# Optimization experiments

Hardware: AMD Instinct MI355X
Metric: run time of the kernel (lower is better)

Reference implementation:

```python
import jax, jax.numpy as jnp
import numpy as np
import math

B, T, XD, H, DD, P = 512, 256, 128, 512, 16, 32
IN = 2 * XD + DD  # GRUCell input size


def _init(key, shape, fan):
    stdv = 1.0 / math.sqrt(fan)
    return jax.random.uniform(key, shape, jnp.float32, -stdv, stdv)


def setup_inputs() -> dict:
    key = jax.random.key(0)
    ks = jax.random.split(key, 32)
    inp = {
        "values": jax.random.normal(ks[0], (B, T, XD), jnp.float32),
        "lens": jnp.full((B,), T, dtype=jnp.int32),  # lens[0] == max_len
        "static": jax.random.normal(ks[1], (B, DD), jnp.float32),
        "times": jax.random.uniform(ks[2], (B, T, XD), jnp.float32),
        "masks": (jax.random.uniform(ks[3], (B, T, XD)) < 0.8).astype(jnp.float32),
        "prototype": jax.random.normal(ks[4], (P, H), jnp.float32),
        "proto": True,
        # temp_decay_h: Linear(x_dim -> hidden), custom uniform(-1/sqrt(H), 1/sqrt(H))
        "Wd": _init(ks[5], (H, XD), H), "bd": _init(ks[6], (H,), XD),
        # hist_reg: Linear(hidden -> x_dim)
        "Wh": _init(ks[7], (XD, H), H), "bh": _init(ks[8], (XD,), H),
        "Wf": _init(ks[9], (XD, XD), XD), "bf": _init(ks[10], (XD,), XD),
        # ProtoAttn Q/K/V: Linear(hidden -> hidden)
        "Wq": _init(ks[11], (H, H), H), "bq": _init(ks[12], (H,), H),
        "Wk": _init(ks[13], (H, H), H), "bk": _init(ks[14], (H,), H),
        "Wv": _init(ks[15], (H, H), H), "bv": _init(ks[16], (H,), H),
        # gating W: Linear(2*hidden -> 1)
        "Wg": _init(ks[17], (1, 2 * H), 2 * H), "bg": _init(ks[18], (1,), 2 * H),
        # GRUCell
        "Wih": _init(ks[19], (3 * H, IN), H), "Whh": _init(ks[20], (3 * H, H), H),
        "bih": _init(ks[21], (3 * H,), H), "bhh": _init(ks[22], (3 * H,), H),
    }
    return inp


def _forward(values, static, times, masks, prototype,
             Wd, bd, Wh, bh, Wf, bf, Wq, bq, Wk, bk, Wv, bv, Wg, bg,
             Wih, Whh, bih, bhh, lens, proto):
    feat_m = 1.0 - jnp.eye(XD, dtype=values.dtype)  # zero-diagonal mask
    gamma = jnp.exp(-jax.nn.relu(jnp.einsum("btx,hx->bth", times, Wd) + bd))
    # attention key/value do not depend on h -> precompute
    keyp = prototype @ Wk.T + bk      # [P,H]
    valp = prototype @ Wv.T + bv      # [P,H]
    scale = 1.0 / math.sqrt(P)
    valid = (jnp.arange(T)[:, None] < lens[None, :]).astype(values.dtype)  # [T,B]

    xs = (jnp.swapaxes(values, 0, 1),  # [T,B,XD]
          jnp.swapaxes(masks, 0, 1),   # [T,B,XD]
          jnp.swapaxes(gamma, 0, 1),   # [T,B,H]
          valid[:, :, None])           # [T,B,1]

    h0 = jnp.zeros((B, H), values.dtype)
    xh0 = jnp.zeros((B, XD), values.dtype)

    def step(carry, xt):
        h, x_h = carry
        x, m, g, v = xt
        if proto:
            q = h @ Wq.T + bq                          # [B,H]
            score = (q @ keyp.T) * scale               # [B,P]
            attn = jax.nn.softmax(score, axis=-1)      # dropout omitted (eval)
            h1 = attn @ valp                           # [B,H]
            alpha = jax.nn.sigmoid(jnp.concatenate([h, h1], axis=1) @ Wg.T + bg)
            h = alpha * h + (1.0 - alpha) * h1
        h = h * g
        x_h = jnp.where(v > 0, h @ Wh.T + bh, x_h)
        x_c = m * x + (1.0 - m) * x_h
        z_h = x_c @ (Wf * feat_m).T + bf
        z_c = m * x + (1.0 - m) * z_h
        inp = jnp.concatenate([z_c, m, static], axis=1)
        gx = inp @ Wih.T + bih
        gh = h @ Whh.T + bhh
        xr, xz, xn = jnp.split(gx, 3, axis=1)
        hr, hz, hn = jnp.split(gh, 3, axis=1)
        r = jax.nn.sigmoid(xr + hr)
        z = jax.nn.sigmoid(xz + hz)
        n = jnp.tanh(xn + r * hn)
        h_new = (1.0 - z) * n + z * h
        h = jnp.where(v > 0, h_new, h)
        return (h, x_h), (h, x_c, z_c)

    (hN, _), (hs, x_cs, z_cs) = jax.lax.scan(step, (h0, xh0), xs)
    hs = jnp.swapaxes(hs, 0, 1)
    x_cs = jnp.swapaxes(x_cs, 0, 1)
    z_cs = jnp.swapaxes(z_cs, 0, 1)
    return hs, hN, x_cs, z_cs


def reference(values, lens, static, times, masks, prototype, proto,
              Wd, bd, Wh, bh, Wf, bf, Wq, bq, Wk, bk, Wv, bv, Wg, bg,
              Wih, Whh, bih, bhh):
    return _forward(values, static, times, masks, prototype,
                    Wd, bd, Wh, bh, Wf, bf, Wq, bq, Wk, bk, Wv, bv, Wg, bg,
                    Wih, Whh, bih, bhh, lens, bool(proto))
```

## Files before the change

kernel.cpp:

```cpp
#include <hip/hip_runtime.h>

#define NB 256
#define NT 1024

#define Bv 512
#define Tv 256
#define XDv 128
#define Hv 512
#define DDv 16
#define Pv 32

typedef short s8 __attribute__((ext_vector_type(8)));
typedef float f4 __attribute__((ext_vector_type(4)));
typedef unsigned long long u64;

#define OFF_KEYP 2048
#define OFF_VALP (OFF_KEYP + 16384)
#define OFF_MF   (OFF_VALP + 16384)
#define OFF_C    (OFF_MF + 16384)
#define OFF_VWG  (OFF_C + 32)
#define OFF_FRG  (OFF_VWG + 32)
#define US_WD   0
#define US_MS   65536
#define US_VP   81920
#define US_WH   98304
#define US_WF   163840
#define US_WHH  180224
#define US_WIH  966656
#define US_END  1409024
#define OFF_H   (OFF_FRG + (US_END/2))

#define OUT_HS  0
#define OUT_HN  (Bv*Tv*Hv)
#define OUT_XCS (OUT_HN + Bv*Hv)
#define OUT_ZCS (OUT_XCS + Bv*Tv*XDv)

struct Smem {
  unsigned short hA[32*520];
  unsigned short tA[32*136];
  unsigned short xcA[32*136];
  unsigned short inpA[32*296];
  unsigned short aA[32*40];
  unsigned short mA[32*136];
  unsigned short xhS[32*128];
  float xvS[32*132];
  float scS[32*34];
  float ghS[3*32*33];
  float gxS[3*32*33];
  float hp32[32*32];
  float al[32], rsm[32], cS[32], vwgS[32];
};

__device__ __forceinline__ unsigned short f2b(float f) {
  union { float f; unsigned int u; } x{f};
  unsigned int r = x.u + 0x7fffu + ((x.u >> 16) & 1u);
  return (unsigned short)(r >> 16);
}
__device__ __forceinline__ float b2f(unsigned short u) {
  union { unsigned int u; float f; } x{(unsigned int)u << 16};
  return x.f;
}
__device__ __forceinline__ float sig_f(float x) { return 1.f / (1.f + __expf(-x)); }
__device__ __forceinline__ float tanh_f(float x) {
  x = fminf(fmaxf(x, -15.f), 15.f);
  float e = __expf(2.f * x);
  return (e - 1.f) / (e + 1.f);
}
__device__ __forceinline__ s8 pack8(const float* p) {
  f4 a = *(const f4*)p; f4 b = *(const f4*)(p + 4);
  s8 r;
  r[0]=(short)f2b(a[0]); r[1]=(short)f2b(a[1]); r[2]=(short)f2b(a[2]); r[3]=(short)f2b(a[3]);
  r[4]=(short)f2b(b[0]); r[5]=(short)f2b(b[1]); r[6]=(short)f2b(b[2]); r[7]=(short)f2b(b[3]);
  return r;
}

__device__ __forceinline__ void gridbar(unsigned int* bar, unsigned int& lgen, int bid) {
  __syncthreads();
  if (threadIdx.x == 0) {
    __threadfence();
    const unsigned int target = ++lgen;
    unsigned int* grp = bar + (bid >> 4)*16;
    const unsigned int a =
        __hip_atomic_fetch_add(grp, 1u, __ATOMIC_ACQ_REL, __HIP_MEMORY_SCOPE_AGENT);
    if (a == 15u) {
      __hip_atomic_store(grp, 0u, __ATOMIC_RELAXED, __HIP_MEMORY_SCOPE_AGENT);
      const unsigned int r =
          __hip_atomic_fetch_add(bar + 384, 1u, __ATOMIC_ACQ_REL, __HIP_MEMORY_SCOPE_AGENT);
      if (r == 15u) {
        __hip_atomic_store(bar + 384, 0u, __ATOMIC_RELAXED, __HIP_MEMORY_SCOPE_AGENT);
        __hip_atomic_store(bar + 400, target, __ATOMIC_RELEASE, __HIP_MEMORY_SCOPE_AGENT);
      }
    }
    while (__hip_atomic_load(bar + 400, __ATOMIC_RELAXED, __HIP_MEMORY_SCOPE_AGENT) < target)
      __builtin_amdgcn_s_sleep(2);
    __threadfence();
  }
  __syncthreads();
}

__device__ __forceinline__ void rgbar_nf(unsigned int* bar, unsigned int& lgen, int rg) {
  __syncthreads();
  if (threadIdx.x == 0) {
    const unsigned int target = ++lgen;
    unsigned int* cnt = bar + 512 + rg*64;
    unsigned int* flg = cnt + 32;
    const unsigned int a =
        __hip_atomic_fetch_add(cnt, 1u, __ATOMIC_RELAXED, __HIP_MEMORY_SCOPE_AGENT);
    if (a == 15u) {
      __hip_atomic_store(cnt, 0u, __ATOMIC_RELAXED, __HIP_MEMORY_SCOPE_AGENT);
      asm volatile("s_waitcnt vmcnt(0)" ::: "memory");
      __hip_atomic_store(flg, target, __ATOMIC_RELAXED, __HIP_MEMORY_SCOPE_AGENT);
    } else {
      while (__hip_atomic_load(flg, __ATOMIC_RELAXED, __HIP_MEMORY_SCOPE_AGENT) < target)
        __builtin_amdgcn_s_sleep(2);
    }
  }
  __syncthreads();
}

#define SWZ(DST, NTILES, KT_, EXPR)                                            \
  { const int tot = (NTILES)*(KT_)*512;                                        \
    for (int f = gtid; f < tot; f += NB*NT) {                                  \
      const int e = f & 7, lane_ = (f >> 3) & 63, rem = f >> 9;                \
      const int kt = rem % (KT_), nt = rem / (KT_);                            \
      const int n = nt*16 + (lane_ & 15);                                      \
      const int k = kt*32 + ((lane_ >> 4) & 3)*8 + e;                          \
      (DST)[f] = f2b((EXPR));                                                  \
    } }

#define MFMA(a,b,c) __builtin_amdgcn_mfma_f32_16x16x32_bf16((a),(b),(c),0,0,0)
#define FRAG(P,idx) (*(const s8*)&(P)[((size_t)(idx))*8])
#define NTST(v,p) __builtin_nontemporal_store((v),(p))

__global__ __launch_bounds__(NT, 4)
void rits_main(const float* __restrict__ values, const int* __restrict__ lens,
               const float* __restrict__ statc, const float* __restrict__ times,
               const float* __restrict__ masks, const float* __restrict__ prototype,
               const int* __restrict__ protoflag,
               const float* __restrict__ Wd, const float* __restrict__ bd,
               const float* __restrict__ Wh, const float* __restrict__ bh,
               const float* __restrict__ Wf, const float* __restrict__ bf,
               const float* __restrict__ Wq, const float* __restrict__ bq,
               const float* __restrict__ Wk, const float* __restrict__ bk,
               const float* __restrict__ Wv, const float* __restrict__ bv,
               const float* __restrict__ Wg, const float* __restrict__ bg,
               const float* __restrict__ Wih, const float* __restrict__ Whh,
               const float* __restrict__ bih, const float* __restrict__ bhh,
               float* __restrict__ out, float* __restrict__ ws)
{
  const int bid = blockIdx.x, tid = threadIdx.x;
  const int gtid = bid*NT + tid;
  const int wv = tid >> 6, ln = tid & 63;
  const int l15 = ln & 15, l4 = ln >> 4;
  const int rg = (bid & 7)*2 + ((bid >> 7) & 1);
  const int cg = (bid >> 3) & 15;
  const int r0 = rg*32, c0 = cg*32;
  unsigned int* bar = (unsigned int*)ws;
  unsigned int lgenG = 0, lgenR = 0;
  unsigned short* frg = (unsigned short*)(ws + OFF_FRG);
  const unsigned short* wdW  = frg + US_WD;
  const unsigned short* msW  = frg + US_MS;
  const unsigned short* vpW  = frg + US_VP;
  const unsigned short* whW  = frg + US_WH;
  const unsigned short* wfW  = frg + US_WF;
  const unsigned short* whhW = frg + US_WHH;
  const unsigned short* wihW = frg + US_WIH;
  unsigned int* wsH = (unsigned int*)(ws + OFF_H);

  __shared__ Smem L;
  const bool proto = protoflag[0] != 0;
  const float scale = 0.17677669529663687f;

  for (int o = gtid; o < 2*Pv*Hv; o += NB*NT) {
    const int which = o >> 14, rem = o & 16383;
    const int p = rem >> 9, j = rem & 511;
    const float* W = which ? Wv : Wk;
    const float* bb = which ? bv : bk;
    const float* pr = prototype + p*Hv;
    const float* wr = W + j*Hv;
    float s = bb[j];
    #pragma unroll 4
    for (int k = 0; k < Hv; ++k) s += pr[k]*wr[k];
    ws[(which ? OFF_VALP : OFF_KEYP) + p*Hv + j] = s;
  }
  SWZ(frg + US_WD, 32, 4,  Wd[n*XDv + k])
  SWZ(frg + US_WH, 8, 16,  Wh[n*Hv + k])
  SWZ(frg + US_WF, 8, 4,   (n == k ? 0.f : Wf[n*XDv + k]))
  SWZ(frg + US_WHH, 96, 16,
      Whh[((size_t)(n >> 9)*Hv + (((n >> 5) & 15)*32 + ((n >> 4) & 1)*16 + (n & 15)))*Hv + k])
  SWZ(frg + US_WIH, 96, 9,
      (k < 272 ? Wih[((size_t)(n >> 9)*Hv + (((n >> 5) & 15)*32 + ((n >> 4) & 1)*16 + (n & 15)))*272 + k] : 0.f))
  gridbar(bar, lgenG, bid);

  {
    const float* keyp = ws + OFF_KEYP;
    const float* valp = ws + OFF_VALP;
    for (int o = gtid; o < Pv*Hv; o += NB*NT) {
      const int p = o >> 9, kc = o & 511;
      float s = 0.f;
      #pragma unroll 4
      for (int j = 0; j < Hv; ++j) s += keyp[p*Hv + j]*Wq[j*Hv + kc];
      ws[OFF_MF + o] = s;
    }
    if (gtid < 32) {
      float s = 0.f;
      for (int j = 0; j < Hv; ++j) s += bq[j]*keyp[gtid*Hv + j];
      ws[OFF_C + gtid] = s;
    } else if (gtid < 64) {
      const int p = gtid - 32;
      float s = 0.f;
      for (int j = 0; j < Hv; ++j) s += valp[p*Hv + j]*Wg[Hv + j];
      ws[OFF_VWG + p] = s;
    }
  }
  gridbar(bar, lgenG, bid);

  SWZ(frg + US_MS, 2, 16, (ws + OFF_MF)[n*Hv + k])
  SWZ(frg + US_VP, 32, 1, (ws + OFF_VALP)[k*Hv + n])
  gridbar(bar, lgenG, bid);

  for (int o = tid; o < 32*128; o += NT) L.xhS[o] = 0;
  if (tid < 32) { L.cS[tid] = ws[OFF_C + tid]; L.vwgS[tid] = ws[OFF_VWG + tid]; }
  for (int o = tid; o < 32*40; o += NT) {
    const int row = o / 40, cc = o % 40;
    L.inpA[row*296 + 256 + cc] =
        (cc < DDv) ? f2b(statc[(r0 + row)*DDv + cc]) : (unsigned short)0;
  }

  const int wrt = wv >> 3;
  const int ws8 = wv & 7;
  const int xcol = ws8*16 + l15;
  const float bhR = bh[xcol], bfR = bf[xcol];
  int lensA[4];
  #pragma unroll
  for (int i = 0; i < 4; ++i)
    lensA[i] = lens[r0 + wrt*16 + l4*4 + i];
  float wgr[8];
  if (wv >= 8) {
    #pragma unroll
    for (int e = 0; e < 8; ++e) wgr[e] = Wg[ln*8 + e];
  }
  f4 bdW;
  #pragma unroll
  for (int q = 0; q < 4; ++q) bdW[q] = bd[ws8*64 + q*16 + l15];
  const int crow = tid >> 5, cjj = tid & 31;
  float bihR[3], bhhR[3];
  #pragma unroll
  for (int g = 0; g < 3; ++g) { bihR[g] = bih[g*Hv + c0 + cjj]; bhhR[g] = bhh[g*Hv + c0 + cjj]; }
  const int lensG0 = lens[r0 + crow];
  const float bg0 = bg[0];

  float pv[4], pm[4], pt[4];
  #pragma unroll
  for (int i = 0; i < 4; ++i) {
    const int o = i*NT + tid, row = o >> 7, col = o & 127;
    const size_t a = ((size_t)(r0 + row)*Tv + 0)*XDv + col;
    pv[i] = values[a]; pm[i] = masks[a]; pt[i] = times[a];
  }
  __syncthreads();

  for (int t = 0; t < Tv; ++t) {
    if (t > 0) {
      const u64* src64 = (const u64*)(wsH + ((t - 1) & 1)*131072) + (size_t)r0*128;
      #pragma unroll
      for (int i = 0; i < 4; ++i) {
        const int o = i*NT + tid, row = o >> 7, cp = o & 127;
        ((u64*)&L.hA[row*520])[cp] = __hip_atomic_load(
            &src64[(size_t)row*128 + cp], __ATOMIC_RELAXED, __HIP_MEMORY_SCOPE_AGENT);
      }
    } else {
      for (int o = tid; o < 32*128; o += NT) {
        const int row = o >> 7, cp = o & 127;
        ((u64*)&L.hA[row*520])[cp] = 0ull;
      }
    }
    #pragma unroll
    for (int i = 0; i < 4; ++i) {
      const int o = i*NT + tid, row = o >> 7, col = o & 127;
      L.xvS[row*132 + col] = pv[i];
      L.mA[row*136 + col]  = f2b(pm[i]);
      L.tA[row*136 + col]  = f2b(pt[i]);
    }
    {
      const int tn = (t + 1 < Tv) ? t + 1 : t;
      #pragma unroll
      for (int i = 0; i < 4; ++i) {
        const int o = i*NT + tid, row = o >> 7, col = o & 127;
        const size_t a = ((size_t)(r0 + row)*Tv + tn)*XDv + col;
        pv[i] = values[a]; pm[i] = masks[a]; pt[i] = times[a];
      }
    }
    __syncthreads();

    if (proto) {
      if (wv < 4) {
        const int rt = wv >> 1, nt = wv & 1;
        f4 acc = {0.f,0.f,0.f,0.f};
        #pragma unroll
        for (int kt = 0; kt < 16; ++kt) {
          s8 a = *(const s8*)&L.hA[(rt*16 + l15)*520 + kt*32 + l4*8];
          acc = MFMA(a, FRAG(msW, (nt*16 + kt)*64 + ln), acc);
        }
        #pragma unroll
        for (int i = 0; i < 4; ++i)
          L.scS[(rt*16 + l4*4 + i)*34 + nt*16 + l15] = acc[i];
      } else if (wv >= 8) {
        #pragma unroll
        for (int rr = 0; rr < 4; ++rr) {
          const int row = (wv - 8)*4 + rr;
          s8 hv8 = *(const s8*)&L.hA[row*520 + ln*8];
          float s = 0.f;
          #pragma unroll
          for (int e = 0; e < 8; ++e) s += b2f((unsigned short)hv8[e]) * wgr[e];
          s += __shfl_xor(s, 1);  s += __shfl_xor(s, 2);  s += __shfl_xor(s, 4);
          s += __shfl_xor(s, 8);  s += __shfl_xor(s, 16); s += __shfl_xor(s, 32);
          if (ln == 0) L.scS[row*34 + 32] = s;
        }
      }
    }
    __syncthreads();

    if (proto && wv == 0 && ln < 32) {
      const int r = ln;
      float mx = -1e30f;
      #pragma unroll 8
      for (int p = 0; p < 32; ++p)
        mx = fmaxf(mx, (L.scS[r*34 + p] + L.cS[p]) * scale);
      float sm = 0.f, a1 = 0.f;
      #pragma unroll 8
      for (int p = 0; p < 32; ++p) {
        float e = __expf((L.scS[r*34 + p] + L.cS[p]) * scale - mx);
        sm += e; a1 += e * L.vwgS[p];
        L.aA[r*40 + p] = f2b(e);
      }
      const float rs = 1.f / sm;
      L.rsm[r] = rs;
      L.al[r] = sig_f(L.scS[r*34 + 32] + a1*rs + bg0);
    }
    __syncthreads();

    {
      s8 ta[4]; s8 aa;
      #pragma unroll
      for (int kt = 0; kt < 4; ++kt)
        ta[kt] = *(const s8*)&L.tA[(wrt*16 + l15)*136 + kt*32 + l4*8];
      if (proto) aa = *(const s8*)&L.aA[(wrt*16 + l15)*40 + l4*8];
      #pragma unroll
      for (int q = 0; q < 4; ++q) {
        const int nt = ws8*4 + q;
        const int col = nt*16 + l15;
        f4 g2 = {0.f,0.f,0.f,0.f};
        #pragma unroll
        for (int kt = 0; kt < 4; ++kt)
          g2 = MFMA(ta[kt], FRAG(wdW, (nt*4 + kt)*64 + ln), g2);
        f4 h12 = {0.f,0.f,0.f,0.f};
        if (proto) h12 = MFMA(aa, FRAG(vpW, nt*64 + ln), h12);
        #pragma unroll
        for (int i = 0; i < 4; ++i) {
          const int row = wrt*16 + l4*4 + i;
          const float gam = __expf(-fmaxf(g2[i] + bdW[q], 0.f));
          const float hbf = b2f(L.hA[row*520 + col]);
          float hp;
          if (proto) {
            const float av = L.al[row];
            hp = (av*hbf + (1.f - av)*h12[i]*L.rsm[row]) * gam;
          } else hp = hbf * gam;
          L.hA[row*520 + col] = f2b(hp);
          const unsigned cc = (unsigned)(col - c0);
          if (cc < 32u) L.hp32[row*32 + cc] = hp;
        }
      }
    }
    __syncthreads();

    {
      const bool doG = ws8 < 6;
      const int g = ws8 >> 1, hf = ws8 & 1;
      const int ntG = g*32 + cg*2 + hf;
      f4 accX = {0.f,0.f,0.f,0.f};
      f4 accG = {0.f,0.f,0.f,0.f};
      #pragma unroll
      for (int kt = 0; kt < 16; ++kt) {
        s8 a = *(const s8*)&L.hA[(wrt*16 + l15)*520 + kt*32 + l4*8];
        accX = MFMA(a, FRAG(whW, (ws8*16 + kt)*64 + ln), accX);
        if (doG) accG = MFMA(a, FRAG(whhW, (ntG*16 + kt)*64 + ln), accG);
      }
      #pragma unroll
      for (int i = 0; i < 4; ++i) {
        const int row = wrt*16 + l4*4 + i;
        const int b = r0 + row;
        float xh = accX[i] + bhR;
        if (t < lensA[i]) L.xhS[row*128 + xcol] = f2b(xh);
        else              xh = b2f(L.xhS[row*128 + xcol]);
        const float xv = L.xvS[row*132 + xcol], mv = b2f(L.mA[row*136 + xcol]);
        const float xc = mv*xv + (1.f - mv)*xh;
        if (cg == 0) NTST(xc, &out[OUT_XCS + ((size_t)b*Tv + t)*XDv + xcol]);
        L.xcA[row*136 + xcol] = f2b(xc);
      }
      if (doG) {
        const int cLoc = hf*16 + l15;
        #pragma unroll
        for (int i = 0; i < 4; ++i)
          L.ghS[g*1056 + (wrt*16 + l4*4 + i)*33 + cLoc] = accG[i];
      }
    }
    __syncthreads();

    {
      f4 acc = {0.f,0.f,0.f,0.f};
      #pragma unroll
      for (int kt = 0; kt < 4; ++kt) {
        s8 a = *(const s8*)&L.xcA[(wrt*16 + l15)*136 + kt*32 + l4*8];
        acc = MFMA(a, FRAG(wfW, (ws8*4 + kt)*64 + ln), acc);
      }
      #pragma unroll
      for (int i = 0; i < 4; ++i) {
        const int row = wrt*16 + l4*4 + i;
        const float xv = L.xvS[row*132 + xcol], mv = b2f(L.mA[row*136 + xcol]);
        const float zc = mv*xv + (1.f - mv)*(acc[i] + bfR);
        if (cg == 0) NTST(zc, &out[OUT_ZCS + ((size_t)(r0 + row)*Tv + t)*XDv + xcol]);
        L.inpA[row*296 + xcol]       = f2b(zc);
        L.inpA[row*296 + 128 + xcol] = f2b(mv);
      }
    }
    __syncthreads();

    if (wv < 12) {
      const int g = wv >> 2, sub = wv & 3;
      const int hf = sub >> 1, rt = sub & 1;
      const int ntG = g*32 + cg*2 + hf;
      const int cLoc = hf*16 + l15;
      f4 acc = {0.f,0.f,0.f,0.f};
      #pragma unroll
      for (int kt = 0; kt < 9; ++kt) {
        s8 a = *(const s8*)&L.inpA[(rt*16 + l15)*296 + kt*32 + l4*8];
        acc = MFMA(a, FRAG(wihW, (ntG*9 + kt)*64 + ln), acc);
      }
      #pragma unroll
      for (int i = 0; i < 4; ++i)
        L.gxS[g*1056 + (rt*16 + l4*4 + i)*33 + cLoc] = acc[i];
    }
    __syncthreads();

    unsigned int* dst = wsH + (t & 1)*131072;
    {
      const int row = crow;
      const int b = r0 + row, jc = c0 + cjj;
      const float xr = L.gxS[row*33 + cjj]        + bihR[0];
      const float xz = L.gxS[1056 + row*33 + cjj] + bihR[1];
      const float xn = L.gxS[2112 + row*33 + cjj] + bihR[2];
      const float hr = L.ghS[row*33 + cjj]        + bhhR[0];
      const float hz = L.ghS[1056 + row*33 + cjj] + bhhR[1];
      const float hn = L.ghS[2112 + row*33 + cjj] + bhhR[2];
      const float r = sig_f(xr + hr), z = sig_f(xz + hz);
      const float n = tanh_f(xn + r*hn);
      const float hpv = L.hp32[row*32 + cjj];
      const float hfv = (t < lensG0) ? ((1.f - z)*n + z*hpv) : hpv;
      NTST(hfv, &out[OUT_HS + ((size_t)b*Tv + t)*Hv + jc]);
      if (t == Tv - 1) NTST(hfv, &out[OUT_HN + (size_t)b*Hv + jc]);
      const float partner = __shfl_xor(hfv, 1);
      if ((cjj & 1) == 0) {
        const unsigned int pk = (unsigned int)f2b(hfv) | ((unsigned int)f2b(partner) << 16);
        __hip_atomic_store(&dst[(size_t)b*256 + cg*16 + (cjj >> 1)], pk,
                           __ATOMIC_RELAXED, __HIP_MEMORY_SCOPE_AGENT);
      }
    }
    rgbar_nf(bar, lgenR, rg);
  }
}

extern "C" void kernel_launch(void* const* d_in, const int* in_sizes, int n_in,
                              void* d_out, int out_size, void* d_ws, size_t ws_size,
                              hipStream_t stream) {
  (void)in_sizes; (void)n_in; (void)out_size; (void)ws_size;
  hipMemsetAsync(d_ws, 0, 8192, stream);
  rits_main<<<NB, NT, 0, stream>>>(
      (const float*)d_in[0],  (const int*)d_in[1],   (const float*)d_in[2],
      (const float*)d_in[3],  (const float*)d_in[4], (const float*)d_in[5],
      (const int*)d_in[6],
      (const float*)d_in[7],  (const float*)d_in[8],
      (const float*)d_in[9],  (const float*)d_in[10],
      (const float*)d_in[11], (const float*)d_in[12],
      (const float*)d_in[13], (const float*)d_in[14],
      (const float*)d_in[15], (const float*)d_in[16],
      (const float*)d_in[17], (const float*)d_in[18],
      (const float*)d_in[19], (const float*)d_in[20],
      (const float*)d_in[21], (const float*)d_in[22],
      (const float*)d_in[23], (const float*)d_in[24],
      (float*)d_out, (float*)d_ws);
}
```

Measured before the change: 14.59 ms.

## Reuse weight fragments across both row tiles and parallelize softmax across warps

Several per-step MFMA stages now have each wave cover both 16-row tiles with one loaded B fragment, instead of splitting row tiles across waves. This halves the weight-fragment loads from registers or LDS. The decay/attention stage and the Wh/Whh stage are redistributed: Wh runs on waves 0-7 and Whh on waves 8-13, so they no longer share a loop. The softmax, previously done serially by 32 lanes of one wave, now runs across all waves using shuffle reductions. In exchange, some stages use fewer waves, which adds per-wave latency and register pressure.

Result: no change. 14.38 ms (-1.4%).

```diff
diff --git a/kernel.cpp b/kernel.cpp
--- a/kernel.cpp
+++ b/kernel.cpp
@@ -227,22 +227,23 @@
         (cc < DDv) ? f2b(statc[(r0 + row)*DDv + cc]) : (unsigned short)0;
   }
 
-  const int wrt = wv >> 3;
-  const int ws8 = wv & 7;
-  const int xcol = ws8*16 + l15;
-  const float bhR = bh[xcol], bfR = bf[xcol];
-  int lensA[4];
+  const int w8 = wv & 7;
+  const int xcol8 = w8*16 + l15;
+  const float bhR = bh[xcol8], bfR = bf[xcol8];
+  int lensB2[8];
   #pragma unroll
-  for (int i = 0; i < 4; ++i)
-    lensA[i] = lens[r0 + wrt*16 + l4*4 + i];
+  for (int rt = 0; rt < 2; ++rt)
+    #pragma unroll
+    for (int i = 0; i < 4; ++i)
+      lensB2[rt*4 + i] = lens[r0 + rt*16 + l4*4 + i];
   float wgr[8];
   if (wv >= 8) {
     #pragma unroll
     for (int e = 0; e < 8; ++e) wgr[e] = Wg[ln*8 + e];
   }
-  f4 bdW;
+  float bdW2[2];
   #pragma unroll
-  for (int q = 0; q < 4; ++q) bdW[q] = bd[ws8*64 + q*16 + l15];
+  for (int q = 0; q < 2; ++q) bdW2[q] = bd[(wv*2 + q)*16 + l15];
   const int crow = tid >> 5, cjj = tid & 31;
   float bihR[3], bhhR[3];
   #pragma unroll
@@ -293,17 +294,22 @@
     __syncthreads();
 
     if (proto) {
-      if (wv < 4) {
-        const int rt = wv >> 1, nt = wv & 1;
-        f4 acc = {0.f,0.f,0.f,0.f};
+      if (wv < 2) {
+        const int nt = wv;
+        f4 acc0 = {0.f,0.f,0.f,0.f}, acc1 = {0.f,0.f,0.f,0.f};
         #pragma unroll
         for (int kt = 0; kt < 16; ++kt) {
-          s8 a = *(const s8*)&L.hA[(rt*16 + l15)*520 + kt*32 + l4*8];
-          acc = MFMA(a, FRAG(msW, (nt*16 + kt)*64 + ln), acc);
-        }
-        #pragma unroll
-        for (int i = 0; i < 4; ++i)
-          L.scS[(rt*16 + l4*4 + i)*34 + nt*16 + l15] = acc[i];
+          s8 b  = FRAG(msW, (nt*16 + kt)*64 + ln);
+          s8 a0 = *(const s8*)&L.hA[(l15)*520 + kt*32 + l4*8];
+          s8 a1 = *(const s8*)&L.hA[(16 + l15)*520 + kt*32 + l4*8];
+          acc0 = MFMA(a0, b, acc0);
+          acc1 = MFMA(a1, b, acc1);
+        }
+        #pragma unroll
+        for (int i = 0; i < 4; ++i) {
+          L.scS[(l4*4 + i)*34 + nt*16 + l15]        = acc0[i];
+          L.scS[(16 + l4*4 + i)*34 + nt*16 + l15]   = acc1[i];
+        }
       } else if (wv >= 8) {
         #pragma unroll
         for (int rr = 0; rr < 4; ++rr) {
@@ -320,107 +326,138 @@
     }
     __syncthreads();
 
-    if (proto && wv == 0 && ln < 32) {
-      const int r = ln;
-      float mx = -1e30f;
-      #pragma unroll 8
-      for (int p = 0; p < 32; ++p)
-        mx = fmaxf(mx, (L.scS[r*34 + p] + L.cS[p]) * scale);
-      float sm = 0.f, a1 = 0.f;
-      #pragma unroll 8
-      for (int p = 0; p < 32; ++p) {
-        float e = __expf((L.scS[r*34 + p] + L.cS[p]) * scale - mx);
-        sm += e; a1 += e * L.vwgS[p];
-        L.aA[r*40 + p] = f2b(e);
-      }
-      const float rs = 1.f / sm;
-      L.rsm[r] = rs;
-      L.al[r] = sig_f(L.scS[r*34 + 32] + a1*rs + bg0);
+    if (proto) {
+      const int row = wv*2 + (ln >> 5);
+      const int p = ln & 31;
+      const float sc = (L.scS[row*34 + p] + L.cS[p]) * scale;
+      float mx = sc;
+      mx = fmaxf(mx, __shfl_xor(mx, 1));  mx = fmaxf(mx, __shfl_xor(mx, 2));
+      mx = fmaxf(mx, __shfl_xor(mx, 4));  mx = fmaxf(mx, __shfl_xor(mx, 8));
+      mx = fmaxf(mx, __shfl_xor(mx, 16));
+      const float e = __expf(sc - mx);
+      float sm = e;
+      sm += __shfl_xor(sm, 1); sm += __shfl_xor(sm, 2); sm += __shfl_xor(sm, 4);
+      sm += __shfl_xor(sm, 8); sm += __shfl_xor(sm, 16);
+      float a1 = e * L.vwgS[p];
+      a1 += __shfl_xor(a1, 1); a1 += __shfl_xor(a1, 2); a1 += __shfl_xor(a1, 4);
+      a1 += __shfl_xor(a1, 8); a1 += __shfl_xor(a1, 16);
+      L.aA[row*40 + p] = f2b(e);
+      if (p == 0) {
+        L.rsm[row] = 1.f / sm;
+        L.al[row] = sig_f(L.scS[row*34 + 32] + a1 / sm + bg0);
+      }
     }
     __syncthreads();
 
     {
-      s8 ta[4]; s8 aa;
-      #pragma unroll
-      for (int kt = 0; kt < 4; ++kt)
-        ta[kt] = *(const s8*)&L.tA[(wrt*16 + l15)*136 + kt*32 + l4*8];
-      if (proto) aa = *(const s8*)&L.aA[(wrt*16 + l15)*40 + l4*8];
-      #pragma unroll
-      for (int q = 0; q < 4; ++q) {
-        const int nt = ws8*4 + q;
+      s8 ta[2][4]; s8 aa[2];
+      #pragma unroll
+      for (int rt = 0; rt < 2; ++rt) {
+        #pragma unroll
+        for (int kt = 0; kt < 4; ++kt)
+          ta[rt][kt] = *(const s8*)&L.tA[(rt*16 + l15)*136 + kt*32 + l4*8];
+        if (proto) aa[rt] = *(const s8*)&L.aA[(rt*16 + l15)*40 + l4*8];
+      }
+      #pragma unroll
+      for (int q = 0; q < 2; ++q) {
+        const int nt = wv*2 + q;
         const int col = nt*16 + l15;
-        f4 g2 = {0.f,0.f,0.f,0.f};
-        #pragma unroll
-        for (int kt = 0; kt < 4; ++kt)
-          g2 = MFMA(ta[kt], FRAG(wdW, (nt*4 + kt)*64 + ln), g2);
-        f4 h12 = {0.f,0.f,0.f,0.f};
-        if (proto) h12 = MFMA(aa, FRAG(vpW, nt*64 + ln), h12);
+        f4 g2[2] = {{0.f,0.f,0.f,0.f},{0.f,0.f,0.f,0.f}};
+        f4 h12[2] = {{0.f,0.f,0.f,0.f},{0.f,0.f,0.f,0.f}};
+        #pragma unroll
+        for (int kt = 0; kt < 4; ++kt) {
+          s8 b = FRAG(wdW, (nt*4 + kt)*64 + ln);
+          g2[0] = MFMA(ta[0][kt], b, g2[0]);
+          g2[1] = MFMA(ta[1][kt], b, g2[1]);
+        }
+        if (proto) {
+          s8 b = FRAG(vpW, nt*64 + ln);
+          h12[0] = MFMA(aa[0], b, h12[0]);
+          h12[1] = MFMA(aa[1], b, h12[1]);
+        }
+        #pragma unroll
+        for (int rt = 0; rt < 2; ++rt) {
+          #pragma unroll
+          for (int i = 0; i < 4; ++i) {
+            const int row = rt*16 + l4*4 + i;
+            const float gam = __expf(-fmaxf(g2[rt][i] + bdW2[q], 0.f));
+            const float hbf = b2f(L.hA[row*520 + col]);
+            float hp;
+            if (proto) {
+              const float av = L.al[row];
+              hp = (av*hbf + (1.f - av)*h12[rt][i]*L.rsm[row]) * gam;
+            } else hp = hbf * gam;
+            L.hA[row*520 + col] = f2b(hp);
+            const unsigned cc = (unsigned)(col - c0);
+            if (cc < 32u) L.hp32[row*32 + cc] = hp;
+          }
+        }
+      }
+    }
+    __syncthreads();
+
+    if (wv < 8) {
+      f4 accX[2] = {{0.f,0.f,0.f,0.f},{0.f,0.f,0.f,0.f}};
+      #pragma unroll
+      for (int kt = 0; kt < 16; ++kt) {
+        s8 b  = FRAG(whW, (wv*16 + kt)*64 + ln);
+        s8 a0 = *(const s8*)&L.hA[(l15)*520 + kt*32 + l4*8];
+        s8 a1 = *(const s8*)&L.hA[(16 + l15)*520 + kt*32 + l4*8];
+        accX[0] = MFMA(a0, b, accX[0]);
+        accX[1] = MFMA(a1, b, accX[1]);
+      }
+      #pragma unroll
+      for (int rt = 0; rt < 2; ++rt) {
         #pragma unroll
         for (int i = 0; i < 4; ++i) {
-          const int row = wrt*16 + l4*4 + i;
-          const float gam = __expf(-fmaxf(g2[i] + bdW[q], 0.f));
-          const float hbf = b2f(L.hA[row*520 + col]);
-          float hp;
-          if (proto) {
-            const float av = L.al[row];
-            hp = (av*hbf + (1.f - av)*h12[i]*L.rsm[row]) * gam;
-          } else hp = hbf * gam;
-          L.hA[row*520 + col] = f2b(hp);
-          const unsigned cc = (unsigned)(col - c0);
-          if (cc < 32u) L.hp32[row*32 + cc] = hp;
-        }
-      }
+          const int row = rt*16 + l4*4 + i;
+          const int b = r0 + row;
+          float xh = accX[rt][i] + bhR;
+          if (t < lensB2[rt*4 + i]) L.xhS[row*128 + xcol8] = f2b(xh);
+          else                      xh = b2f(L.xhS[row*128 + xcol8]);
+          const float xv = L.xvS[row*132 + xcol8], mv = b2f(L.mA[row*136 + xcol8]);
+          const float xc = mv*xv + (1.f - mv)*xh;
+          if (cg == 0) NTST(xc, &out[OUT_XCS + ((size_t)b*Tv + t)*XDv + xcol8]);
+          L.xcA[row*136 + xcol8] = f2b(xc);
+        }
+      }
+    } else if (wv < 14) {
+      const int j = wv - 8, g = j >> 1, hf = j & 1;
+      const int ntG = g*32 + cg*2 + hf;
+      const int cLoc = hf*16 + l15;
+      f4 accG[2] = {{0.f,0.f,0.f,0.f},{0.f,0.f,0.f,0.f}};
+      #pragma unroll
+      for (int kt = 0; kt < 16; ++kt) {
+        s8 b  = FRAG(whhW, (ntG*16 + kt)*64 + ln);
+        s8 a0 = *(const s8*)&L.hA[(l15)*520 + kt*32 + l4*8];
+        s8 a1 = *(const s8*)&L.hA[(16 + l15)*520 + kt*32 + l4*8];
+        accG[0] = MFMA(a0, b, accG[0]);
+        accG[1] = MFMA(a1, b, accG[1]);
+      }
+      #pragma unroll
+      for (int rt = 0; rt < 2; ++rt)
+        #pragma unroll
+        for (int i = 0; i < 4; ++i)
+          L.ghS[g*1056 + (rt*16 + l4*4 + i)*33 + cLoc] = accG[rt][i];
     }
     __syncthreads();
 
     {
-      const bool doG = ws8 < 6;
-      const int g = ws8 >> 1, hf = ws8 & 1;
-      const int ntG = g*32 + cg*2 + hf;
-      f4 accX = {0.f,0.f,0.f,0.f};
-      f4 accG = {0.f,0.f,0.f,0.f};
-      #pragma unroll
-      for (int kt = 0; kt < 16; ++kt) {
-        s8 a = *(const s8*)&L.hA[(wrt*16 + l15)*520 + kt*32 + l4*8];
-        accX = MFMA(a, FRAG(whW, (ws8*16 + kt)*64 + ln), accX);
-        if (doG) accG = MFMA(a, FRAG(whhW, (ntG*16 + kt)*64 + ln), accG);
+      const int wrt = wv >> 3;
+      f4 acc = {0.f,0.f,0.f,0.f};
+      #pragma unroll
+      for (int kt = 0; kt < 4; ++kt) {
+        s8 a = *(const s8*)&L.xcA[(wrt*16 + l15)*136 + kt*32 + l4*8];
+        acc = MFMA(a, FRAG(wfW, (w8*4 + kt)*64 + ln), acc);
       }
       #pragma unroll
       for (int i = 0; i < 4; ++i) {
         const int row = wrt*16 + l4*4 + i;
-        const int b = r0 + row;
-        float xh = accX[i] + bhR;
-        if (t < lensA[i]) L.xhS[row*128 + xcol] = f2b(xh);
-        else              xh = b2f(L.xhS[row*128 + xcol]);
-        const float xv = L.xvS[row*132 + xcol], mv = b2f(L.mA[row*136 + xcol]);
-        const float xc = mv*xv + (1.f - mv)*xh;
-        if (cg == 0) NTST(xc, &out[OUT_XCS + ((size_t)b*Tv + t)*XDv + xcol]);
-        L.xcA[row*136 + xcol] = f2b(xc);
-      }
-      if (doG) {
-        const int cLoc = hf*16 + l15;
-        #pragma unroll
-        for (int i = 0; i < 4; ++i)
-          L.ghS[g*1056 + (wrt*16 + l4*4 + i)*33 + cLoc] = accG[i];
-      }
-    }
-    __syncthreads();
-
-    {
-      f4 acc = {0.f,0.f,0.f,0.f};
-      #pragma unroll
-      for (int kt = 0; kt < 4; ++kt) {
-        s8 a = *(const s8*)&L.xcA[(wrt*16 + l15)*136 + kt*32 + l4*8];
-        acc = MFMA(a, FRAG(wfW, (ws8*4 + kt)*64 + ln), acc);
-      }
-      #pragma unroll
-      for (int i = 0; i < 4; ++i) {
-        const int row = wrt*16 + l4*4 + i;
-        const float xv = L.xvS[row*132 + xcol], mv = b2f(L.mA[row*136 + xcol]);
+        const float xv = L.xvS[row*132 + xcol8], mv = b2f(L.mA[row*136 + xcol8]);
         const float zc = mv*xv + (1.f - mv)*(acc[i] + bfR);
-        if (cg == 0) NTST(zc, &out[OUT_ZCS + ((size_t)(r0 + row)*Tv + t)*XDv + xcol]);
-        L.inpA[row*296 + xcol]       = f2b(zc);
-        L.inpA[row*296 + 128 + xcol] = f2b(mv);
+        if (cg == 0) NTST(zc, &out[OUT_ZCS + ((size_t)(r0 + row)*Tv + t)*XDv + xcol8]);
+        L.inpA[row*296 + xcol8]       = f2b(zc);
+        L.inpA[row*296 + 128 + xcol8] = f2b(mv);
       }
     }
     __syncthreads();
```
